# Kernel optimization log

Hardware: AMD Instinct MI355X
Metric: run time of the kernel (lower is better)

Reference implementation:

```python
import jax, jax.numpy as jnp
import numpy as np

T, B, D, N = 2048, 16, 1024, 64
EPS = 1e-6


def setup_inputs() -> dict:
    key = jax.random.key(0)
    k1, k2 = jax.random.split(key)
    x = jax.random.normal(k1, (T, B, D), dtype=jnp.float32)
    S0 = jnp.zeros((B, N, N), dtype=jnp.float32)
    # xavier-uniform-ish scale for each [N, D] block of the fused projection
    limit = float(np.sqrt(6.0 / (N + D)))
    W_kvqg = jax.random.uniform(k2, (4 * N, D), dtype=jnp.float32, minval=-limit, maxval=limit)
    b_gate = jnp.full((N,), 2.0, dtype=jnp.float32)
    return {"x": x, "S0": S0, "W_kvqg": W_kvqg, "b_gate": b_gate}


def _silu(z):
    return z * jax.nn.sigmoid(z)


def reference(x, S0, W_kvqg, b_gate):
    n = b_gate.shape[0]
    # fused projection: [T, B, 4n]
    proj = jnp.einsum('tbd,nd->tbn', x, W_kvqg)
    k_all = proj[..., :n]
    v_all = proj[..., n:2 * n]
    q_all = proj[..., 2 * n:3 * n]
    g_all = proj[..., 3 * n:]

    def step(S, inp):
        k, v, q, g = inp
        decay = jax.nn.sigmoid(g + b_gate)                      # [B, n]
        k_norm = k / (jnp.linalg.norm(k, axis=-1, keepdims=True) + EPS)
        retrieved = jnp.einsum('bij,bj->bi', S, k_norm)         # [B, n]
        delta = v - retrieved
        S = decay[:, :, None] * S + delta[:, :, None] * k_norm[:, None, :]
        Sq = jnp.einsum('bij,bj->bi', S, q)                     # [B, n]
        out = Sq * _silu(Sq)
        return S, out

    S_final, output = jax.lax.scan(step, S0, (k_all, v_all, q_all, g_all))
    return output, S_final
```

## Files before the change

### kernel.cpp

```cpp
#include <hip/hip_runtime.h>
#include <hip/hip_bf16.h>
#include <math.h>

#define T_STEPS 2048
#define B_SZ 16
#define D_SZ 1024
#define N_SZ 64
#define M_ROWS (T_STEPS * B_SZ)
#define NOUT (4 * N_SZ)
#define U_BLK 8
#define NBLK (T_STEPS / U_BLK)
#define TSTR 17

typedef __attribute__((ext_vector_type(8))) short bf16x8;
typedef __attribute__((ext_vector_type(4))) float f32x4;

template <int CTRL, int RMASK, bool BC>
__device__ __forceinline__ float dpp_add(float v) {
  return v + __int_as_float(__builtin_amdgcn_update_dpp(
                 0, __float_as_int(v), CTRL, RMASK, 0xF, BC));
}
__device__ __forceinline__ float wave_red(float v) {
  v = dpp_add<0xB1, 0xF, true>(v);
  v = dpp_add<0x4E, 0xF, true>(v);
  v = dpp_add<0x141, 0xF, true>(v);
  v = dpp_add<0x140, 0xF, true>(v);
  v = dpp_add<0x142, 0xA, false>(v);
  v = dpp_add<0x143, 0xC, false>(v);
  return __int_as_float(__builtin_amdgcn_readlane(__float_as_int(v), 63));
}

__device__ __forceinline__ unsigned cvt2(float a, float b) {
  float2 f; f.x = a; f.y = b;
  __hip_bfloat162 h = __float22bfloat162_rn(f);
  return *reinterpret_cast<unsigned*>(&h);
}

__global__ __launch_bounds__(256) void wcvt(const float* __restrict__ W,
                                            unsigned* __restrict__ Wb) {
  const size_t idx = ((size_t)blockIdx.x * 256 + threadIdx.x) * 4;
  const float4 f = *reinterpret_cast<const float4*>(&W[idx]);
  uint2 o;
  o.x = cvt2(f.x, f.y);
  o.y = cvt2(f.z, f.w);
  *reinterpret_cast<uint2*>(&Wb[idx >> 1]) = o;
}

__global__ __launch_bounds__(256) void gemm_proj(const float* __restrict__ x,
                                                 const unsigned short* __restrict__ Wb,
                                                 float* __restrict__ proj) {
  __shared__ unsigned short Al[64][72];
  __shared__ unsigned short Bl[256][72];
  const int tid = threadIdx.x;
  const int lane = tid & 63;
  const int wv = tid >> 6;
  const int m0 = blockIdx.x * 64;
  const int nw0 = wv * 64;

  f32x4 acc[4][4];
#pragma unroll
  for (int m = 0; m < 4; ++m)
#pragma unroll
    for (int n = 0; n < 4; ++n) acc[m][n] = (f32x4){0.f, 0.f, 0.f, 0.f};

  const int arow = tid >> 2;
  const int akb = (tid & 3) * 16;

  for (int k0 = 0; k0 < D_SZ; k0 += 64) {
    {
      const float* src = &x[(size_t)(m0 + arow) * D_SZ + k0 + akb];
      unsigned tmp[8];
#pragma unroll
      for (int c = 0; c < 4; ++c) {
        const float4 f = *reinterpret_cast<const float4*>(src + c * 4);
        tmp[2 * c] = cvt2(f.x, f.y);
        tmp[2 * c + 1] = cvt2(f.z, f.w);
      }
      *reinterpret_cast<float4*>(&Al[arow][akb]) =
          *reinterpret_cast<const float4*>(&tmp[0]);
      *reinterpret_cast<float4*>(&Al[arow][akb + 8]) =
          *reinterpret_cast<const float4*>(&tmp[4]);
    }
    {
      const unsigned short* src = &Wb[(size_t)tid * D_SZ + k0];
#pragma unroll
      for (int h = 0; h < 8; ++h)
        *reinterpret_cast<float4*>(&Bl[tid][h * 8]) =
            *reinterpret_cast<const float4*>(&src[h * 8]);
    }
    __syncthreads();
    const int fr = lane & 15;
#pragma unroll
    for (int kk = 0; kk < 64; kk += 32) {
      const int kof = kk + (lane >> 4) * 8;
      bf16x8 af[4], bfr[4];
#pragma unroll
      for (int m = 0; m < 4; ++m)
        af[m] = *reinterpret_cast<const bf16x8*>(&Al[m * 16 + fr][kof]);
#pragma unroll
      for (int n = 0; n < 4; ++n)
        bfr[n] = *reinterpret_cast<const bf16x8*>(&Bl[nw0 + n * 16 + fr][kof]);
#pragma unroll
      for (int m = 0; m < 4; ++m)
#pragma unroll
        for (int n = 0; n < 4; ++n)
          acc[m][n] = __builtin_amdgcn_mfma_f32_16x16x32_bf16(
              af[m], bfr[n], acc[m][n], 0, 0, 0);
    }
    __syncthreads();
  }

  const int col = lane & 15;
  const int rb = (lane >> 4) * 4;
#pragma unroll
  for (int m = 0; m < 4; ++m)
#pragma unroll
    for (int n = 0; n < 4; ++n)
#pragma unroll
      for (int r = 0; r < 4; ++r)
        proj[(size_t)(m0 + m * 16 + rb + r) * NOUT + nw0 + n * 16 + col] =
            acc[m][n][r];
}

__global__ __launch_bounds__(512) void norm_gram(float* __restrict__ proj,
                                                 const float* __restrict__ b_gate,
                                                 float* __restrict__ gram) {
  const int u = threadIdx.x >> 6;
  const int lane = threadIdx.x & 63;
  const int grp = blockIdx.x;
  const int blk = grp & (NBLK - 1);
  const int b = grp >> 8;
  const int t0 = blk * U_BLK;
  const int m = (t0 + u) * B_SZ + b;

  __shared__ float lds_kn[U_BLK][64];

  float* p = proj + (size_t)m * NOUT;
  const float kf = p[lane];
  const float vf = p[64 + lane];
  const float qf = p[128 + lane];
  const float gf = p[192 + lane];
  const float bg = b_gate[lane];
  const float ss = wave_red(kf * kf);
  const float kn = kf / (sqrtf(ss) + 1e-6f);
  const float dec = 1.f / (1.f + expf(-(gf + bg)));
  asm volatile("s_waitcnt vmcnt(0)" ::: "memory");
  float2* pp = reinterpret_cast<float2*>(p);
  float2 a; a.x = kn; a.y = qf;
  float2 c; c.x = vf; c.y = dec;
  pp[lane] = a;
  pp[64 + lane] = c;

  lds_kn[u][lane] = kn;
  __syncthreads();

  float row[8];
#pragma unroll
  for (int cc = 0; cc < 8; ++cc) {
    const float knc = lds_kn[cc][lane];
    const float lhs = (cc > u) ? kn : qf;
    row[cc] = wave_red(lhs * knc);
  }
  if (lane == 0) {
    float* dst = gram + ((size_t)grp * 64 + u * 8);
    float4 r0, r1;
    r0.x = row[0]; r0.y = row[1]; r0.z = row[2]; r0.w = row[3];
    r1.x = row[4]; r1.y = row[5]; r1.z = row[6]; r1.w = row[7];
    *reinterpret_cast<float4*>(dst) = r0;
    *reinterpret_cast<float4*>(dst + 4) = r1;
  }
}

__global__ __launch_bounds__(256, 1) void scan_kernel(
    const float* __restrict__ proj, const float* __restrict__ gram,
    const float* __restrict__ S0, float* __restrict__ out,
    float* __restrict__ Sfin) {
  const int wid = threadIdx.x >> 6;
  const int lane = threadIdx.x & 63;
  const int bid = blockIdx.x;
  const int b = (bid & 7) | ((bid >> 7) << 3);
  const int i = (((bid >> 3) & 15) << 2) | wid;

  __shared__ float ldsT[2][64 * TSTR];
  __shared__ float ldsV[2][U_BLK * 128];
  __shared__ float ldsG[2][64];
  __shared__ float ldsS[4][64];

  float S = S0[(size_t)b * 4096 + i * 64 + lane];

  const int r0 = wid * 2;
  float4 st0, st1;
  float stg = 0.f;

#define STAGE_LOAD(blkv)                                                      \
  {                                                                           \
    const size_t g0 = ((size_t)(((blkv) * U_BLK + r0) * B_SZ + b)) * NOUT;    \
    st0 = *reinterpret_cast<const float4*>(&proj[g0 + lane * 4]);             \
    st1 = *reinterpret_cast<const float4*>(&proj[g0 + (size_t)B_SZ * NOUT +   \
                                                 lane * 4]);                  \
    if (wid == 0) stg = gram[((size_t)b * NBLK + (blkv)) * 64 + lane];        \
  }

#define STAGE_WRITE(bufv)                                                     \
  {                                                                           \
    if (lane < 32) {                                                          \
      const int j0 = lane * 2;                                                \
      ldsT[bufv][j0 * TSTR + r0] = st0.x;                                     \
      ldsT[bufv][j0 * TSTR + 8 + r0] = st0.y;                                 \
      ldsT[bufv][(j0 + 1) * TSTR + r0] = st0.z;                               \
      ldsT[bufv][(j0 + 1) * TSTR + 8 + r0] = st0.w;                           \
      ldsT[bufv][j0 * TSTR + r0 + 1] = st1.x;                                 \
      ldsT[bufv][j0 * TSTR + 8 + r0 + 1] = st1.y;                             \
      ldsT[bufv][(j0 + 1) * TSTR + r0 + 1] = st1.z;                           \
      ldsT[bufv][(j0 + 1) * TSTR + 8 + r0 + 1] = st1.w;                       \
    } else {                                                                  \
      *reinterpret_cast<float4*>(                                             \
          &ldsV[bufv][r0 * 128 + (lane - 32) * 4]) = st0;                     \
      *reinterpret_cast<float4*>(                                             \
          &ldsV[bufv][(r0 + 1) * 128 + (lane - 32) * 4]) = st1;               \
    }                                                                         \
    if (wid == 0) ldsG[bufv][lane] = stg;                                     \
  }

#define GM(idx) __int_as_float(                                               \
    __builtin_amdgcn_readlane(__float_as_int(gv), (idx)))

  STAGE_LOAD(0)
  STAGE_WRITE(0)
  __syncthreads();

  const int koff = (lane >> 4) * 8;
  const int col = lane & 15;

  for (int blk = 0; blk < NBLK; ++blk) {
    const int buf = blk & 1;
    if (blk + 1 < NBLK) STAGE_LOAD(blk + 1)

    ldsS[wid][lane] = S;
    asm volatile("s_waitcnt lgkmcnt(0)" ::: "memory");

    float2 vdv[8];
#pragma unroll
    for (int u = 0; u < 8; ++u)
      vdv[u] = *reinterpret_cast<const float2*>(&ldsV[buf][u * 128 + i * 2]);
    const float gv = ldsG[buf][lane];
    float knl[8];
#pragma unroll
    for (int w = 0; w < 8; ++w) knl[w] = ldsT[buf][lane * TSTR + w];

    f32x4 red = (f32x4){0.f, 0.f, 0.f, 0.f};
#pragma unroll
    for (int kk = 0; kk < 2; ++kk) {
      float a[8], bsrc[8];
      *reinterpret_cast<float4*>(&a[0]) = *reinterpret_cast<const float4*>(
          &ldsS[wid][kk * 32 + koff]);
      *reinterpret_cast<float4*>(&a[4]) = *reinterpret_cast<const float4*>(
          &ldsS[wid][kk * 32 + koff + 4]);
#pragma unroll
      for (int t = 0; t < 8; ++t)
        bsrc[t] = ldsT[buf][(kk * 32 + koff + t) * TSTR + col];
      union { unsigned u[4]; bf16x8 v; } cvA, cvB;
#pragma unroll
      for (int h = 0; h < 4; ++h) {
        asm("v_cvt_pk_bf16_f32 %0, %1, %2"
            : "=v"(cvA.u[h]) : "v"(a[2 * h]), "v"(a[2 * h + 1]));
        asm("v_cvt_pk_bf16_f32 %0, %1, %2"
            : "=v"(cvB.u[h]) : "v"(bsrc[2 * h]), "v"(bsrc[2 * h + 1]));
      }
      red = __builtin_amdgcn_mfma_f32_16x16x32_bf16(cvA.v, cvB.v, red, 0, 0, 0);
    }

    float c[9], rc[8];
    c[0] = 1.f;
#pragma unroll
    for (int u = 0; u < 8; ++u) {
      c[u + 1] = c[u] * vdv[u].y;
      rc[u] = __builtin_amdgcn_rcpf(c[u + 1]);
    }

    float acc[8], sac[8];
    const int ri = __float_as_int(red[0]);
#pragma unroll
    for (int u = 0; u < 8; ++u) {
      acc[u] = __int_as_float(__builtin_amdgcn_readlane(ri, u));
      sac[u] = __int_as_float(__builtin_amdgcn_readlane(ri, 8 + u));
    }

    float dp[8], sqv[8];
#pragma unroll
    for (int w = 0; w < 8; ++w) {
      const float d = fmaf(-c[w], acc[w], vdv[w].x);
      dp[w] = d * rc[w];
      sqv[w] = fmaf(c[w + 1], sac[w], d * GM(w * 8 + w));
#pragma unroll
      for (int u = w + 1; u < 8; ++u) {
        acc[u] = fmaf(dp[w], GM(w * 8 + u), acc[u]);
        sac[u] = fmaf(dp[w], GM(u * 8 + w), sac[u]);
      }
    }
    float tacc = S;
#pragma unroll
    for (int w = 0; w < 8; ++w) tacc = fmaf(dp[w], knl[w], tacc);
    S = c[8] * tacc;

    if (lane < 8) {
      const float a0 = (lane & 1) ? sqv[1] : sqv[0];
      const float a1 = (lane & 1) ? sqv[3] : sqv[2];
      const float a2 = (lane & 1) ? sqv[5] : sqv[4];
      const float a3 = (lane & 1) ? sqv[7] : sqv[6];
      const float b0 = (lane & 2) ? a1 : a0;
      const float b1 = (lane & 2) ? a3 : a2;
      const float sq = (lane & 4) ? b1 : b0;
      const size_t ob = (size_t)blk * U_BLK * (B_SZ * N_SZ) + b * N_SZ + i;
      out[ob + (size_t)lane * (B_SZ * N_SZ)] =
          sq * sq * __fdividef(1.f, 1.f + __expf(-sq));
    }

    if (blk + 1 < NBLK) STAGE_WRITE(buf ^ 1)
    __syncthreads();
  }

  Sfin[(size_t)b * 4096 + i * 64 + lane] = S;
#undef STAGE_LOAD
#undef STAGE_WRITE
#undef GM
}

extern "C" void kernel_launch(void* const* d_in, const int* in_sizes, int n_in,
                              void* d_out, int out_size, void* d_ws, size_t ws_size,
                              hipStream_t stream) {
  const float* x      = (const float*)d_in[0];
  const float* S0     = (const float*)d_in[1];
  const float* W      = (const float*)d_in[2];
  const float* b_gate = (const float*)d_in[3];
  float* out  = (float*)d_out;
  float* proj = (float*)d_ws;
  float* gram = (float*)((char*)d_ws + (size_t)M_ROWS * NOUT * 4);
  unsigned* Wb = (unsigned*)((char*)d_ws + 35u * 1024 * 1024);

  hipLaunchKernelGGL(wcvt, dim3(256), dim3(256), 0, stream, W, Wb);
  hipLaunchKernelGGL(gemm_proj, dim3(M_ROWS / 64), dim3(256), 0, stream,
                     x, (const unsigned short*)Wb, proj);
  hipLaunchKernelGGL(norm_gram, dim3(B_SZ * NBLK), dim3(512), 0, stream,
                     proj, b_gate, gram);
  hipLaunchKernelGGL(scan_kernel, dim3(256), dim3(256), 0, stream,
                     proj, gram, S0, out, out + (size_t)T_STEPS * B_SZ * N_SZ);
}
```

Baseline: 324.1 us.

## Process two state rows per wave in scan kernel, halving block count

```diff
diff --git a/kernel.cpp b/kernel.cpp
--- a/kernel.cpp
+++ b/kernel.cpp
@@ -178,15 +178,18 @@
   const int wid = threadIdx.x >> 6;
   const int lane = threadIdx.x & 63;
   const int bid = blockIdx.x;
-  const int b = (bid & 7) | ((bid >> 7) << 3);
-  const int i = (((bid >> 3) & 15) << 2) | wid;
+  const int b = (bid & 7) | ((bid >> 6) << 3);
+  const int ig = (bid >> 3) & 7;
+  const int i0 = ig * 8 + wid * 2;
+  const int i1 = i0 + 1;
 
   __shared__ float ldsT[2][64 * TSTR];
   __shared__ float ldsV[2][U_BLK * 128];
   __shared__ float ldsG[2][64];
-  __shared__ float ldsS[4][64];
-
-  float S = S0[(size_t)b * 4096 + i * 64 + lane];
+  __shared__ float ldsS[4][2][64];
+
+  float Sa = S0[(size_t)b * 4096 + i0 * 64 + lane];
+  float Sb = S0[(size_t)b * 4096 + i1 * 64 + lane];
 
   const int r0 = wid * 2;
   float4 st0, st1;
@@ -236,83 +239,120 @@
     const int buf = blk & 1;
     if (blk + 1 < NBLK) STAGE_LOAD(blk + 1)
 
-    ldsS[wid][lane] = S;
+    ldsS[wid][0][lane] = Sa;
+    ldsS[wid][1][lane] = Sb;
     asm volatile("s_waitcnt lgkmcnt(0)" ::: "memory");
 
-    float2 vdv[8];
-#pragma unroll
-    for (int u = 0; u < 8; ++u)
-      vdv[u] = *reinterpret_cast<const float2*>(&ldsV[buf][u * 128 + i * 2]);
+    float2 vdvA[8], vdvB[8];
+#pragma unroll
+    for (int u = 0; u < 8; ++u) {
+      vdvA[u] = *reinterpret_cast<const float2*>(&ldsV[buf][u * 128 + i0 * 2]);
+      vdvB[u] = *reinterpret_cast<const float2*>(&ldsV[buf][u * 128 + i1 * 2]);
+    }
     const float gv = ldsG[buf][lane];
     float knl[8];
 #pragma unroll
     for (int w = 0; w < 8; ++w) knl[w] = ldsT[buf][lane * TSTR + w];
 
-    f32x4 red = (f32x4){0.f, 0.f, 0.f, 0.f};
+    f32x4 redA = (f32x4){0.f, 0.f, 0.f, 0.f};
+    f32x4 redB = (f32x4){0.f, 0.f, 0.f, 0.f};
 #pragma unroll
     for (int kk = 0; kk < 2; ++kk) {
-      float a[8], bsrc[8];
-      *reinterpret_cast<float4*>(&a[0]) = *reinterpret_cast<const float4*>(
-          &ldsS[wid][kk * 32 + koff]);
-      *reinterpret_cast<float4*>(&a[4]) = *reinterpret_cast<const float4*>(
-          &ldsS[wid][kk * 32 + koff + 4]);
+      float aA[8], aB[8], bsrc[8];
+      *reinterpret_cast<float4*>(&aA[0]) = *reinterpret_cast<const float4*>(
+          &ldsS[wid][0][kk * 32 + koff]);
+      *reinterpret_cast<float4*>(&aA[4]) = *reinterpret_cast<const float4*>(
+          &ldsS[wid][0][kk * 32 + koff + 4]);
+      *reinterpret_cast<float4*>(&aB[0]) = *reinterpret_cast<const float4*>(
+          &ldsS[wid][1][kk * 32 + koff]);
+      *reinterpret_cast<float4*>(&aB[4]) = *reinterpret_cast<const float4*>(
+          &ldsS[wid][1][kk * 32 + koff + 4]);
 #pragma unroll
       for (int t = 0; t < 8; ++t)
         bsrc[t] = ldsT[buf][(kk * 32 + koff + t) * TSTR + col];
-      union { unsigned u[4]; bf16x8 v; } cvA, cvB;
+      union { unsigned u[4]; bf16x8 v; } cvAa, cvAb, cvB;
 #pragma unroll
       for (int h = 0; h < 4; ++h) {
         asm("v_cvt_pk_bf16_f32 %0, %1, %2"
-            : "=v"(cvA.u[h]) : "v"(a[2 * h]), "v"(a[2 * h + 1]));
+            : "=v"(cvAa.u[h]) : "v"(aA[2 * h]), "v"(aA[2 * h + 1]));
+        asm("v_cvt_pk_bf16_f32 %0, %1, %2"
+            : "=v"(cvAb.u[h]) : "v"(aB[2 * h]), "v"(aB[2 * h + 1]));
         asm("v_cvt_pk_bf16_f32 %0, %1, %2"
             : "=v"(cvB.u[h]) : "v"(bsrc[2 * h]), "v"(bsrc[2 * h + 1]));
       }
-      red = __builtin_amdgcn_mfma_f32_16x16x32_bf16(cvA.v, cvB.v, red, 0, 0, 0);
-    }
-
-    float c[9], rc[8];
-    c[0] = 1.f;
+      redA = __builtin_amdgcn_mfma_f32_16x16x32_bf16(cvAa.v, cvB.v, redA, 0, 0, 0);
+      redB = __builtin_amdgcn_mfma_f32_16x16x32_bf16(cvAb.v, cvB.v, redB, 0, 0, 0);
+    }
+
+    float accA[8], sacA[8], accB[8], sacB[8];
+    const int riA = __float_as_int(redA[0]);
+    const int riB = __float_as_int(redB[0]);
 #pragma unroll
     for (int u = 0; u < 8; ++u) {
-      c[u + 1] = c[u] * vdv[u].y;
-      rc[u] = __builtin_amdgcn_rcpf(c[u + 1]);
-    }
-
-    float acc[8], sac[8];
-    const int ri = __float_as_int(red[0]);
+      accA[u] = __int_as_float(__builtin_amdgcn_readlane(riA, u));
+      sacA[u] = __int_as_float(__builtin_amdgcn_readlane(riA, 8 + u));
+      accB[u] = __int_as_float(__builtin_amdgcn_readlane(riB, u));
+      sacB[u] = __int_as_float(__builtin_amdgcn_readlane(riB, 8 + u));
+    }
+
+    float cA[9], rcA[8], cB[9], rcB[8];
+    cA[0] = 1.f; cB[0] = 1.f;
 #pragma unroll
     for (int u = 0; u < 8; ++u) {
-      acc[u] = __int_as_float(__builtin_amdgcn_readlane(ri, u));
-      sac[u] = __int_as_float(__builtin_amdgcn_readlane(ri, 8 + u));
-    }
-
-    float dp[8], sqv[8];
+      cA[u + 1] = cA[u] * vdvA[u].y;
+      rcA[u] = __builtin_amdgcn_rcpf(cA[u + 1]);
+      cB[u + 1] = cB[u] * vdvB[u].y;
+      rcB[u] = __builtin_amdgcn_rcpf(cB[u + 1]);
+    }
+
+    float dpA[8], sqvA[8], dpB[8], sqvB[8];
 #pragma unroll
     for (int w = 0; w < 8; ++w) {
-      const float d = fmaf(-c[w], acc[w], vdv[w].x);
-      dp[w] = d * rc[w];
-      sqv[w] = fmaf(c[w + 1], sac[w], d * GM(w * 8 + w));
+      const float gd = GM(w * 8 + w);
+      const float dA = fmaf(-cA[w], accA[w], vdvA[w].x);
+      dpA[w] = dA * rcA[w];
+      sqvA[w] = fmaf(cA[w + 1], sacA[w], dA * gd);
+      const float dB = fmaf(-cB[w], accB[w], vdvB[w].x);
+      dpB[w] = dB * rcB[w];
+      sqvB[w] = fmaf(cB[w + 1], sacB[w], dB * gd);
 #pragma unroll
       for (int u = w + 1; u < 8; ++u) {
-        acc[u] = fmaf(dp[w], GM(w * 8 + u), acc[u]);
-        sac[u] = fmaf(dp[w], GM(u * 8 + w), sac[u]);
+        const float gG = GM(w * 8 + u);
+        const float gH = GM(u * 8 + w);
+        accA[u] = fmaf(dpA[w], gG, accA[u]);
+        sacA[u] = fmaf(dpA[w], gH, sacA[u]);
+        accB[u] = fmaf(dpB[w], gG, accB[u]);
+        sacB[u] = fmaf(dpB[w], gH, sacB[u]);
       }
     }
-    float tacc = S;
-#pragma unroll
-    for (int w = 0; w < 8; ++w) tacc = fmaf(dp[w], knl[w], tacc);
-    S = c[8] * tacc;
-
-    if (lane < 8) {
-      const float a0 = (lane & 1) ? sqv[1] : sqv[0];
-      const float a1 = (lane & 1) ? sqv[3] : sqv[2];
-      const float a2 = (lane & 1) ? sqv[5] : sqv[4];
-      const float a3 = (lane & 1) ? sqv[7] : sqv[6];
+    float taccA = Sa, taccB = Sb;
+#pragma unroll
+    for (int w = 0; w < 8; ++w) {
+      taccA = fmaf(dpA[w], knl[w], taccA);
+      taccB = fmaf(dpB[w], knl[w], taccB);
+    }
+    Sa = cA[8] * taccA;
+    Sb = cB[8] * taccB;
+
+    if (lane < 16) {
+      const float a0 = (lane & 1) ? sqvA[1] : sqvA[0];
+      const float a1 = (lane & 1) ? sqvA[3] : sqvA[2];
+      const float a2 = (lane & 1) ? sqvA[5] : sqvA[4];
+      const float a3 = (lane & 1) ? sqvA[7] : sqvA[6];
       const float b0 = (lane & 2) ? a1 : a0;
       const float b1 = (lane & 2) ? a3 : a2;
-      const float sq = (lane & 4) ? b1 : b0;
-      const size_t ob = (size_t)blk * U_BLK * (B_SZ * N_SZ) + b * N_SZ + i;
-      out[ob + (size_t)lane * (B_SZ * N_SZ)] =
+      const float sA = (lane & 4) ? b1 : b0;
+      const float e0 = (lane & 1) ? sqvB[1] : sqvB[0];
+      const float e1 = (lane & 1) ? sqvB[3] : sqvB[2];
+      const float e2 = (lane & 1) ? sqvB[5] : sqvB[4];
+      const float e3 = (lane & 1) ? sqvB[7] : sqvB[6];
+      const float f0 = (lane & 2) ? e1 : e0;
+      const float f1 = (lane & 2) ? e3 : e2;
+      const float sB = (lane & 4) ? f1 : f0;
+      const float sq = (lane & 8) ? sB : sA;
+      const int ii = i0 + ((lane >> 3) & 1);
+      const size_t ob = (size_t)blk * U_BLK * (B_SZ * N_SZ) + b * N_SZ + ii;
+      out[ob + (size_t)(lane & 7) * (B_SZ * N_SZ)] =
           sq * sq * __fdividef(1.f, 1.f + __expf(-sq));
     }
 
@@ -320,7 +360,8 @@
     __syncthreads();
   }
 
-  Sfin[(size_t)b * 4096 + i * 64 + lane] = S;
+  Sfin[(size_t)b * 4096 + i0 * 64 + lane] = Sa;
+  Sfin[(size_t)b * 4096 + i1 * 64 + lane] = Sb;
 #undef STAGE_LOAD
 #undef STAGE_WRITE
 #undef GM
@@ -343,6 +384,6 @@
                      x, (const unsigned short*)Wb, proj);
   hipLaunchKernelGGL(norm_gram, dim3(B_SZ * NBLK), dim3(512), 0, stream,
                      proj, b_gate, gram);
-  hipLaunchKernelGGL(scan_kernel, dim3(256), dim3(256), 0, stream,
+  hipLaunchKernelGGL(scan_kernel, dim3(128), dim3(256), 0, stream,
                      proj, gram, S0, out, out + (size_t)T_STEPS * B_SZ * N_SZ);
 }
```

Result: slower. 412.0 us (+27.1%).
